# Optimization experiments

Measured on AMD Instinct MI355X. Metric: run time of the kernel, lower is better.

## Reference

```python
import jax, jax.numpy as jnp
import numpy as np

B, N1, N2, D, R = 4, 128, 128, 256, 4


def setup_inputs() -> dict:
    key = jax.random.key(0)
    ks = jax.random.split(key, 8)
    s = 0.02  # small init scale for weights
    return {
        "features1": jax.random.normal(ks[0], (B, N1, D), jnp.float32),
        "features2": jax.random.normal(ks[1], (B, N2, D), jnp.float32),
        # relation nets stacked over R: Linear(2D->D), Linear(D->D//2), Linear(D//2->1)
        "W1": jax.random.normal(ks[2], (R, 2 * D, D), jnp.float32) * s,
        "b1": jnp.zeros((R, D), jnp.float32),
        "W2": jax.random.normal(ks[3], (R, D, D // 2), jnp.float32) * s,
        "b2": jnp.zeros((R, D // 2), jnp.float32),
        "w3": jax.random.normal(ks[4], (R, D // 2), jnp.float32) * s,
        "b3": jnp.zeros((R,), jnp.float32),
        # aggregator: Linear(D*R -> 2D), Linear(2D -> D)
        "Wa1": jax.random.normal(ks[5], (D * R, 2 * D), jnp.float32) * s,
        "ba1": jnp.zeros((2 * D,), jnp.float32),
        "Wa2": jax.random.normal(ks[6], (2 * D, D), jnp.float32) * s,
        "ba2": jnp.zeros((D,), jnp.float32),
    }


def reference(features1, features2, W1, b1, W2, b2, w3, b3, Wa1, ba1, Wa2, ba2):
    b, n1, d = features1.shape
    n2 = features2.shape[1]
    r = W1.shape[0]
    # concat([f1_i, f2_j]) @ W1 == f1_i @ W1[:d] + f2_j @ W1[d:]
    W1a, W1b = W1[:, :d, :], W1[:, d:, :]
    h1 = jnp.einsum('bid,rde->brie', features1, W1a)          # [B,R,N1,D]
    h2 = jnp.einsum('bjd,rde->brje', features2, W1b)          # [B,R,N2,D]
    h = jax.nn.relu(h1[:, :, :, None, :] + h2[:, :, None, :, :]
                    + b1[None, :, None, None, :])             # [B,R,N1,N2,D]
    g = jax.nn.relu(jnp.einsum('brijd,rde->brije', h, W2)
                    + b2[None, :, None, None, :])             # [B,R,N1,N2,D//2]
    scores = jnp.einsum('brije,re->brij', g, w3) + b3[None, :, None, None]
    w = jax.nn.softmax(scores, axis=-1)                       # softmax over j (N2)
    rel = jnp.einsum('brij,bjd->brid', w, features2)          # [B,R,N1,D]
    # torch cat over relations along feature dim -> relation index outermost
    all_rel = rel.transpose(0, 2, 1, 3).reshape(b, n1, r * d)  # [B,N1,R*D]
    out = jax.nn.relu(all_rel @ Wa1 + ba1) @ Wa2 + ba2         # [B,N1,D]
    return out
```

## Files before the change

### kernel.cpp

```cpp
#include <hip/hip_runtime.h>


typedef _Float16 f16x8 __attribute__((ext_vector_type(8)));
typedef float f32x16 __attribute__((ext_vector_type(16)));

static __device__ __forceinline__ ushort to_h(float f) {
  _Float16 h = (_Float16)f;
  return __builtin_bit_cast(ushort, h);
}
static __device__ __forceinline__ uint pack2(float a, float b) {
  return (uint)to_h(a) | ((uint)to_h(b) << 16);
}
static __device__ __forceinline__ uint pk_add(uint a, uint b) {
  uint r;
  asm("v_pk_add_f16 %0, %1, %2" : "=v"(r) : "v"(a), "v"(b));
  return r;
}
static __device__ __forceinline__ uint pk_relu(uint a) {
  uint r;
  asm("v_pk_max_f16 %0, %1, %2" : "=v"(r) : "v"(a), "v"(0u));
  return r;
}

__global__ __launch_bounds__(256) void k_prep(
    const float* __restrict__ f1, const float* __restrict__ f2,
    const float* __restrict__ W1, const float* __restrict__ W2,
    const float* __restrict__ Wa1, const float* __restrict__ Wa2,
    uint* __restrict__ f1hp, uint* __restrict__ f2hp,
    ushort* __restrict__ W1swz, ushort* __restrict__ W2swz,
    ushort* __restrict__ f2swz, ushort* __restrict__ Wa1swz,
    ushort* __restrict__ Wa2swz)
{
  int blk = blockIdx.x, t = threadIdx.x;
  if (blk < 128) {
    int u = blk * 256 + t;
    float4 a = *(const float4*)&f1[u * 4];
    float4 b = *(const float4*)&f2[u * 4];
    *(uint2*)&f1hp[u * 2] = make_uint2(pack2(a.x, a.y), pack2(a.z, a.w));
    *(uint2*)&f2hp[u * 2] = make_uint2(pack2(b.x, b.y), pack2(b.z, b.w));
    return;
  }
  if (blk < 256) {
    int unit = blk - 128;
    int r = unit >> 5, half = (unit >> 4) & 1, ks = unit & 15;
    int l = t & 63, ctq = t >> 6;
    #pragma unroll
    for (int ci = 0; ci < 2; ++ci) {
      int ct = ctq + ci * 4;
      int e = ct * 32 + (l & 31);
      ushort us[8];
      #pragma unroll
      for (int j = 0; j < 8; ++j) {
        int d = ks * 16 + ((l >> 5) * 4) + (j & 3) + ((j >> 2) * 8);
        us[j] = to_h(W1[(size_t)(r * 512 + half * 256 + d) * 256 + e]);
      }
      uint4 pk;
      pk.x = (uint)us[0] | ((uint)us[1] << 16);
      pk.y = (uint)us[2] | ((uint)us[3] << 16);
      pk.z = (uint)us[4] | ((uint)us[5] << 16);
      pk.w = (uint)us[6] | ((uint)us[7] << 16);
      *(uint4*)&W1swz[(size_t)((((r * 2 + half) * 16 + ks) * 8 + ct) * 64 + l) * 8] = pk;
    }
    return;
  }
  if (blk < 272) {
    int sub = blk - 256;
    int r = sub >> 2, ks0 = (sub & 3) * 4;
    int ct = t >> 6, l = t & 63;
    #pragma unroll
    for (int ko = 0; ko < 4; ++ko) {
      int ks = ks0 + ko;
      ushort us[8];
      #pragma unroll
      for (int j = 0; j < 8; ++j) {
        int d = ks * 16 + ((j >> 2) * 8) + ((l >> 5) * 4) + (j & 3);
        int e = ct * 32 + (l & 31);
        us[j] = to_h(W2[(r * 256 + d) * 128 + e]);
      }
      uint4 pk;
      pk.x = (uint)us[0] | ((uint)us[1] << 16);
      pk.y = (uint)us[2] | ((uint)us[3] << 16);
      pk.z = (uint)us[4] | ((uint)us[5] << 16);
      pk.w = (uint)us[6] | ((uint)us[7] << 16);
      *(uint4*)&W2swz[(((r * 16 + ks) * 4 + ct) * 64 + l) * 8] = pk;
    }
    return;
  }
  if (blk < 288) {
    int sub = blk - 272;
    int w = t >> 6, l = t & 63;
    #pragma unroll
    for (int ko = 0; ko < 4; ++ko) {
      int u = sub * 16 + w * 4 + ko;
      int b = u >> 6, ks = (u >> 3) & 7, ctg = u & 7;
      ushort us[8];
      #pragma unroll
      for (int j = 0; j < 8; ++j) {
        int k = ks * 16 + ((l >> 5) * 4) + (j & 3) + ((j >> 2) * 8);
        int n = ctg * 32 + (l & 31);
        us[j] = to_h(f2[((size_t)b * 128 + k) * 256 + n]);
      }
      uint4 pk;
      pk.x = (uint)us[0] | ((uint)us[1] << 16);
      pk.y = (uint)us[2] | ((uint)us[3] << 16);
      pk.z = (uint)us[4] | ((uint)us[5] << 16);
      pk.w = (uint)us[6] | ((uint)us[7] << 16);
      *(uint4*)&f2swz[(((b * 8 + ks) * 8 + ctg) * 64 + l) * 8] = pk;
    }
    return;
  }
  if (blk < 304) {
    int sub = blk - 288;
    #pragma unroll
    for (int ko = 0; ko < 16; ++ko) {
      int id = sub * 4096 + ko * 256 + t;
      int ks = id >> 10, ct = (id >> 6) & 15, l = id & 63;
      ushort us[8];
      #pragma unroll
      for (int j = 0; j < 8; ++j) {
        int d = ks * 16 + ((l >> 5) * 4) + (j & 3) + ((j >> 2) * 8);
        int e = ct * 32 + (l & 31);
        us[j] = to_h(Wa1[(size_t)d * 512 + e]);
      }
      uint4 pk;
      pk.x = (uint)us[0] | ((uint)us[1] << 16);
      pk.y = (uint)us[2] | ((uint)us[3] << 16);
      pk.z = (uint)us[4] | ((uint)us[5] << 16);
      pk.w = (uint)us[6] | ((uint)us[7] << 16);
      *(uint4*)&Wa1swz[(size_t)id * 8] = pk;
    }
    return;
  }
  {
    int sub = blk - 304;
    #pragma unroll
    for (int ko = 0; ko < 4; ++ko) {
      int id = sub * 1024 + ko * 256 + t;
      int ks = id >> 9, ct = (id >> 6) & 7, l = id & 63;
      ushort us[8];
      #pragma unroll
      for (int j = 0; j < 8; ++j) {
        int d = ks * 16 + ((l >> 5) * 4) + (j & 3) + ((j >> 2) * 8);
        int e = ct * 32 + (l & 31);
        us[j] = to_h(Wa2[(size_t)d * 256 + e]);
      }
      uint4 pk;
      pk.x = (uint)us[0] | ((uint)us[1] << 16);
      pk.y = (uint)us[2] | ((uint)us[3] << 16);
      pk.z = (uint)us[4] | ((uint)us[5] << 16);
      pk.w = (uint)us[6] | ((uint)us[7] << 16);
      *(uint4*)&Wa2swz[(size_t)id * 8] = pk;
    }
    return;
  }
}

__global__ __launch_bounds__(256) void k_proj_mfma(
    const uint* __restrict__ f1hp, const uint* __restrict__ f2hp,
    const ushort* __restrict__ W1swz, const float* __restrict__ b1,
    ushort* __restrict__ h1p, ushort* __restrict__ h2)
{
  int bid = blockIdx.x;
  int it = bid & 3;
  int half = (bid >> 2) & 1;
  int r = (bid >> 3) & 3;
  int b = bid >> 5;
  int t = threadIdx.x, w = t >> 6, l = t & 63;
  __shared__ uint Au[32][132];

  const uint* src = (half ? f2hp : f1hp) + (size_t)b * 16384 + it * 32 * 128;
  #pragma unroll
  for (int q = 0; q < 4; ++q) {
    int lin = q * 256 + t;
    int row = lin >> 5, c4 = (lin & 31) * 4;
    *(uint4*)&Au[row][c4] = *(const uint4*)&src[row * 128 + c4];
  }
  __syncthreads();

  int m31 = l & 31, hi = l >> 5, hi2 = hi * 2;
  f32x16 acc0, acc1;
  #pragma unroll
  for (int e = 0; e < 16; ++e) { acc0[e] = 0.f; acc1[e] = 0.f; }

  const ushort* bb = W1swz + (size_t)(r * 2 + half) * 65536;
  for (int ks = 0; ks < 16; ++ks) {
    int u0 = ks * 8 + hi2;
    uint2 xa = *(const uint2*)&Au[m31][u0];
    uint2 xb = *(const uint2*)&Au[m31][u0 + 4];
    uint4 a4 = make_uint4(xa.x, xa.y, xb.x, xb.y);
    f16x8 af = __builtin_bit_cast(f16x8, a4);
    uint4 br0 = *(const uint4*)&bb[((ks * 8 + w * 2 + 0) * 64 + l) * 8];
    uint4 br1 = *(const uint4*)&bb[((ks * 8 + w * 2 + 1) * 64 + l) * 8];
    f16x8 bf0 = __builtin_bit_cast(f16x8, br0);
    f16x8 bf1 = __builtin_bit_cast(f16x8, br1);
    acc0 = __builtin_amdgcn_mfma_f32_32x32x16_f16(af, bf0, acc0, 0, 0, 0);
    acc1 = __builtin_amdgcn_mfma_f32_32x32x16_f16(af, bf1, acc1, 0, 0, 0);
  }

  ushort* ho = (half ? h2 : h1p) + ((size_t)((b * 4 + r) * 128 + it * 32)) * 256;
  #pragma unroll
  for (int ctl = 0; ctl < 2; ++ctl) {
    int e = (w * 2 + ctl) * 32 + m31;
    float bv = half ? 0.f : b1[r * 256 + e];
    #pragma unroll
    for (int g = 0; g < 16; ++g) {
      int row = (g & 3) + 8 * (g >> 2) + 4 * hi;
      ho[row * 256 + e] = to_h((ctl ? acc1[g] : acc0[g]) + bv);
    }
  }
}

__global__ __launch_bounds__(256, 4) void k_scores_mfma(
    const ushort* __restrict__ h1p, const ushort* __restrict__ h2,
    const ushort* __restrict__ W2swz, const float* __restrict__ b2,
    const float* __restrict__ w3, const float* __restrict__ b3,
    float* __restrict__ scores)
{
  int bid = blockIdx.x;
  int jt = bid & 7;
  int it = (bid >> 3) & 15;
  int r  = (bid >> 7) & 3;
  int b  = bid >> 9;
  int t = threadIdx.x, w = t >> 6, l = t & 63;
  __shared__ uint h1u[8][132];
  __shared__ uint h2u[16][132];
  __shared__ float xch[4][2][2][16];

  const uint* h1g = (const uint*)h1p + ((size_t)((b * 4 + r) * 128 + it * 8)) * 128;
  const uint* h2g = (const uint*)h2  + ((size_t)((b * 4 + r) * 128 + jt * 16)) * 128;
  {
    int row = t >> 5, c4 = (t & 31) * 4;
    *(uint4*)&h1u[row][c4] = *(const uint4*)&h1g[row * 128 + c4];
    *(uint4*)&h2u[row][c4] = *(const uint4*)&h2g[row * 128 + c4];
    *(uint4*)&h2u[row + 8][c4] = *(const uint4*)&h2g[(row + 8) * 128 + c4];
  }

  f32x16 acc[2][2];
  #pragma unroll
  for (int i = 0; i < 2; ++i)
    #pragma unroll
    for (int c = 0; c < 2; ++c)
      #pragma unroll
      for (int e = 0; e < 16; ++e) acc[i][c][e] = 0.f;

  int rtp = w & 1, ctp = w >> 1;
  int hi2 = (l >> 5) * 2;
  int m31 = l & 31;
  int jrow = m31 & 15;
  int irow0 = (rtp * 2 + 0) * 2 + (m31 >> 4);
  int irow1 = (rtp * 2 + 1) * 2 + (m31 >> 4);
  const ushort* bptr = W2swz + r * (16 * 4 * 64 * 8) + (((ctp * 2) * 64 + l) * 8);

  __syncthreads();

  const uint* h1r0 = &h1u[irow0][0];
  const uint* h1r1 = &h1u[irow1][0];
  const uint* h2r  = &h2u[jrow][0];
  uint4 nb0 = *(const uint4*)&bptr[0];
  uint4 nb1 = *(const uint4*)&bptr[512];
  #pragma unroll 2
  for (int ks = 0; ks < 16; ++ks) {
    uint4 b0 = nb0, b1 = nb1;
    if (ks < 15) {
      nb0 = *(const uint4*)&bptr[(ks + 1) * 2048];
      nb1 = *(const uint4*)&bptr[(ks + 1) * 2048 + 512];
    }
    int u0 = ks * 8 + hi2;
    uint2 ya  = *(const uint2*)&h2r[u0];
    uint2 yb  = *(const uint2*)&h2r[u0 + 4];
    uint2 xa0 = *(const uint2*)&h1r0[u0];
    uint2 xb0 = *(const uint2*)&h1r0[u0 + 4];
    uint2 xa1 = *(const uint2*)&h1r1[u0];
    uint2 xb1 = *(const uint2*)&h1r1[u0 + 4];
    uint4 pk0, pk1;
    pk0.x = pk_relu(pk_add(xa0.x, ya.x));
    pk0.y = pk_relu(pk_add(xa0.y, ya.y));
    pk0.z = pk_relu(pk_add(xb0.x, yb.x));
    pk0.w = pk_relu(pk_add(xb0.y, yb.y));
    pk1.x = pk_relu(pk_add(xa1.x, ya.x));
    pk1.y = pk_relu(pk_add(xa1.y, ya.y));
    pk1.z = pk_relu(pk_add(xb1.x, yb.x));
    pk1.w = pk_relu(pk_add(xb1.y, yb.y));
    f16x8 af0 = __builtin_bit_cast(f16x8, pk0);
    f16x8 af1 = __builtin_bit_cast(f16x8, pk1);
    f16x8 bf0 = __builtin_bit_cast(f16x8, b0);
    f16x8 bf1 = __builtin_bit_cast(f16x8, b1);
    acc[0][0] = __builtin_amdgcn_mfma_f32_32x32x16_f16(af0, bf0, acc[0][0], 0, 0, 0);
    acc[0][1] = __builtin_amdgcn_mfma_f32_32x32x16_f16(af0, bf1, acc[0][1], 0, 0, 0);
    acc[1][0] = __builtin_amdgcn_mfma_f32_32x32x16_f16(af1, bf0, acc[1][0], 0, 0, 0);
    acc[1][1] = __builtin_amdgcn_mfma_f32_32x32x16_f16(af1, bf1, acc[1][1], 0, 0, 0);
  }

  float sp[2][16];
  #pragma unroll
  for (int i = 0; i < 2; ++i)
    #pragma unroll
    for (int g = 0; g < 16; ++g) sp[i][g] = 0.f;
  #pragma unroll
  for (int ctl = 0; ctl < 2; ++ctl) {
    int e = (ctp * 2 + ctl) * 32 + m31;
    float w3v = w3[r * 128 + e];
    float b2v = b2[r * 128 + e];
    #pragma unroll
    for (int i = 0; i < 2; ++i)
      #pragma unroll
      for (int g = 0; g < 16; ++g)
        sp[i][g] = fmaf(w3v, fmaxf(acc[i][ctl][g] + b2v, 0.f), sp[i][g]);
  }
  #pragma unroll
  for (int off = 16; off >= 1; off >>= 1)
    #pragma unroll
    for (int i = 0; i < 2; ++i)
      #pragma unroll
      for (int g = 0; g < 16; ++g)
        sp[i][g] += __shfl_xor(sp[i][g], off, 64);
  int hi = l >> 5;
  if (m31 == 0) {
    #pragma unroll
    for (int i = 0; i < 2; ++i)
      #pragma unroll
      for (int g = 0; g < 16; ++g)
        xch[w][i][hi][g] = sp[i][g];
  }
  __syncthreads();
  if (w < 2 && m31 == 0) {
    float b3v = b3[r];
    float* sc_base = scores + (((b * 4 + r) * 128 + it * 8) * 128) + jt * 16;
    #pragma unroll
    for (int i = 0; i < 2; ++i)
      #pragma unroll
      for (int g = 0; g < 16; ++g) {
        float s = xch[w][i][hi][g] + xch[w + 2][i][hi][g] + b3v;
        int p = (w * 2 + i) * 32 + (g & 3) + 8 * (g >> 2) + hi * 4;
        sc_base[(p >> 4) * 128 + (p & 15)] = s;
      }
  }
}

__global__ __launch_bounds__(64, 1) void k_softrel_mfma(
    const float* __restrict__ scores, const ushort* __restrict__ f2swz,
    ushort* __restrict__ all_rel_h)
{
  int bid = blockIdx.x;
  int ctp  = bid & 1;
  int rowq = (bid >> 1) & 3;
  int nh   = (bid >> 3) & 1;
  int r    = (bid >> 4) & 3;
  int b    = bid >> 6;
  int l = threadIdx.x;
  int row = rowq * 32 + (l & 31);
  const float* srow = scores + ((size_t)(b * 4 + r) * 128 + row) * 128;

  float p[128];
  #pragma unroll
  for (int q = 0; q < 32; ++q) {
    float4 v = *(const float4*)&srow[q * 4];
    p[q * 4 + 0] = v.x; p[q * 4 + 1] = v.y;
    p[q * 4 + 2] = v.z; p[q * 4 + 3] = v.w;
  }
  float mm[8];
  #pragma unroll
  for (int c = 0; c < 8; ++c) mm[c] = p[c * 16];
  #pragma unroll
  for (int k = 1; k < 16; ++k)
    #pragma unroll
    for (int c = 0; c < 8; ++c) mm[c] = fmaxf(mm[c], p[c * 16 + k]);
  float m = fmaxf(fmaxf(fmaxf(mm[0], mm[1]), fmaxf(mm[2], mm[3])),
                  fmaxf(fmaxf(mm[4], mm[5]), fmaxf(mm[6], mm[7])));
  float ss[8];
  #pragma unroll
  for (int c = 0; c < 8; ++c) ss[c] = 0.f;
  #pragma unroll
  for (int k = 0; k < 16; ++k)
    #pragma unroll
    for (int c = 0; c < 8; ++c) {
      p[c * 16 + k] = __expf(p[c * 16 + k] - m);
      ss[c] += p[c * 16 + k];
    }
  float sum = ((ss[0] + ss[1]) + (ss[2] + ss[3])) + ((ss[4] + ss[5]) + (ss[6] + ss[7]));
  float inv = 1.f / sum;
  uint preg[64];
  #pragma unroll
  for (int q = 0; q < 64; ++q)
    preg[q] = pack2(p[2 * q] * inv, p[2 * q + 1] * inv);

  f32x16 acc[2];
  #pragma unroll
  for (int c = 0; c < 2; ++c)
    #pragma unroll
    for (int e = 0; e < 16; ++e) acc[c][e] = 0.f;

  int hi2 = (l >> 5) * 2;
  const ushort* bbase = f2swz + (size_t)b * (8 * 8 * 64 * 8);
  #pragma unroll
  for (int ks = 0; ks < 8; ++ks) {
    int b2i = ks * 8 + hi2;
    uint4 pk = make_uint4(preg[b2i], preg[b2i + 1], preg[b2i + 4], preg[b2i + 5]);
    f16x8 af = __builtin_bit_cast(f16x8, pk);
    #pragma unroll
    for (int ctl = 0; ctl < 2; ++ctl) {
      int ct = nh * 4 + ctp * 2 + ctl;
      uint4 braw = *(const uint4*)&bbase[((ks * 8 + ct) * 64 + l) * 8];
      f16x8 bfr = __builtin_bit_cast(f16x8, braw);
      acc[ctl] = __builtin_amdgcn_mfma_f32_32x32x16_f16(af, bfr, acc[ctl], 0, 0, 0);
    }
  }

  ushort* dst = all_rel_h + (size_t)(b * 128) * 1024;
  int ebase = r * 256 + nh * 128 + ctp * 64 + (l & 31);
  int half4 = (l >> 5) << 2;
  #pragma unroll
  for (int ctl = 0; ctl < 2; ++ctl)
    #pragma unroll
    for (int g = 0; g < 16; ++g) {
      int i = rowq * 32 + (g & 3) + 8 * (g >> 2) + half4;
      dst[(size_t)i * 1024 + ebase + ctl * 32] = to_h(acc[ctl][g]);
    }
}

__global__ __launch_bounds__(256) void k_mlp1(
    const ushort* __restrict__ all_rel_h, const ushort* __restrict__ Wa1swz,
    const float* __restrict__ ba1, ushort* __restrict__ hiddenh)
{
  int cq = blockIdx.x, rt = blockIdx.y;
  int t = threadIdx.x, w = t >> 6, l = t & 63;
  __shared__ uint Ah[32][514];
  const uint* Ag = (const uint*)all_rel_h + (size_t)rt * 32 * 512;
  #pragma unroll
  for (int q = 0; q < 16; ++q) {
    int lin = q * 256 + t;
    int row = lin >> 7, c4 = (lin & 127) * 4;
    *(uint4*)&Ah[row][c4] = *(const uint4*)&Ag[row * 512 + c4];
  }
  __syncthreads();

  int m31 = l & 31, hi = l >> 5, hi2 = hi * 2;
  int ct = cq * 4 + w;
  f32x16 acc;
  #pragma unroll
  for (int e = 0; e < 16; ++e) acc[e] = 0.f;
  for (int ks = 0; ks < 64; ++ks) {
    int u0 = ks * 8 + hi2;
    uint2 xa = *(const uint2*)&Ah[m31][u0];
    uint2 xb = *(const uint2*)&Ah[m31][u0 + 4];
    uint4 a4 = make_uint4(xa.x, xa.y, xb.x, xb.y);
    f16x8 af = __builtin_bit_cast(f16x8, a4);
    uint4 braw = *(const uint4*)&Wa1swz[(size_t)((ks * 16 + ct) * 64 + l) * 8];
    f16x8 bfr = __builtin_bit_cast(f16x8, braw);
    acc = __builtin_amdgcn_mfma_f32_32x32x16_f16(af, bfr, acc, 0, 0, 0);
  }
  int e = ct * 32 + m31;
  float bv = ba1[e];
  #pragma unroll
  for (int g = 0; g < 16; ++g) {
    int row = (g & 3) + 8 * (g >> 2) + 4 * hi;
    hiddenh[(size_t)(rt * 32 + row) * 512 + e] = to_h(fmaxf(acc[g] + bv, 0.f));
  }
}

__global__ __launch_bounds__(256) void k_mlp2(
    const ushort* __restrict__ hiddenh, const ushort* __restrict__ Wa2swz,
    const float* __restrict__ ba2, float* __restrict__ out)
{
  int cq = blockIdx.x, rt = blockIdx.y;
  int t = threadIdx.x, w = t >> 6, l = t & 63;
  __shared__ uint Ah[32][258];
  const uint* Ag = (const uint*)hiddenh + (size_t)rt * 32 * 256;
  #pragma unroll
  for (int q = 0; q < 8; ++q) {
    int lin = q * 256 + t;
    int row = lin >> 6, c4 = (lin & 63) * 4;
    *(uint4*)&Ah[row][c4] = *(const uint4*)&Ag[row * 256 + c4];
  }
  __syncthreads();

  int m31 = l & 31, hi = l >> 5, hi2 = hi * 2;
  int ct = cq * 4 + w;
  f32x16 acc;
  #pragma unroll
  for (int e = 0; e < 16; ++e) acc[e] = 0.f;
  for (int ks = 0; ks < 32; ++ks) {
    int u0 = ks * 8 + hi2;
    uint2 xa = *(const uint2*)&Ah[m31][u0];
    uint2 xb = *(const uint2*)&Ah[m31][u0 + 4];
    uint4 a4 = make_uint4(xa.x, xa.y, xb.x, xb.y);
    f16x8 af = __builtin_bit_cast(f16x8, a4);
    uint4 braw = *(const uint4*)&Wa2swz[(size_t)((ks * 8 + ct) * 64 + l) * 8];
    f16x8 bfr = __builtin_bit_cast(f16x8, braw);
    acc = __builtin_amdgcn_mfma_f32_32x32x16_f16(af, bfr, acc, 0, 0, 0);
  }
  int e = ct * 32 + m31;
  float bv = ba2[e];
  #pragma unroll
  for (int g = 0; g < 16; ++g) {
    int row = (g & 3) + 8 * (g >> 2) + 4 * hi;
    out[(size_t)(rt * 32 + row) * 256 + e] = acc[g] + bv;
  }
}

extern "C" void kernel_launch(void* const* d_in, const int* in_sizes, int n_in,
                              void* d_out, int out_size, void* d_ws, size_t ws_size,
                              hipStream_t stream) {
  const float* f1  = (const float*)d_in[0];
  const float* f2  = (const float*)d_in[1];
  const float* W1  = (const float*)d_in[2];
  const float* b1  = (const float*)d_in[3];
  const float* W2  = (const float*)d_in[4];
  const float* b2  = (const float*)d_in[5];
  const float* w3  = (const float*)d_in[6];
  const float* b3  = (const float*)d_in[7];
  const float* Wa1 = (const float*)d_in[8];
  const float* ba1 = (const float*)d_in[9];
  const float* Wa2 = (const float*)d_in[10];
  const float* ba2 = (const float*)d_in[11];
  float* out = (float*)d_out;
  float* ws = (float*)d_ws;

  uint*   f1hp     = (uint*)ws;
  uint*   f2hp     = (uint*)(ws + 65536);
  ushort* h1p      = (ushort*)(ws + 131072);
  ushort* h2       = (ushort*)(ws + 393216);
  float*  scores   = ws + 655360;
  ushort* all_relh = (ushort*)(ws + 917504);
  ushort* W1swz    = (ushort*)(ws + 1179648);
  ushort* W2swz    = (ushort*)(ws + 1441792);
  ushort* f2swz    = (ushort*)(ws + 1507328);
  ushort* Wa1swz   = (ushort*)(ws + 1572864);
  ushort* Wa2swz   = (ushort*)(ws + 1835008);
  ushort* hiddenh  = (ushort*)(ws + 1900544);

  hipLaunchKernelGGL(k_prep, dim3(320), dim3(256), 0, stream,
                     f1, f2, W1, W2, Wa1, Wa2,
                     f1hp, f2hp, W1swz, W2swz, f2swz, Wa1swz, Wa2swz);
  hipLaunchKernelGGL(k_proj_mfma, dim3(128), dim3(256), 0, stream,
                     f1hp, f2hp, W1swz, b1, h1p, h2);
  hipLaunchKernelGGL(k_scores_mfma, dim3(2048), dim3(256), 0, stream,
                     h1p, h2, W2swz, b2, w3, b3, scores);
  hipLaunchKernelGGL(k_softrel_mfma, dim3(256), dim3(64), 0, stream,
                     scores, f2swz, all_relh);
  hipLaunchKernelGGL(k_mlp1, dim3(4, 16), dim3(256), 0, stream,
                     all_relh, Wa1swz, ba1, hiddenh);
  hipLaunchKernelGGL(k_mlp2, dim3(2, 16), dim3(256), 0, stream,
                     hiddenh, Wa2swz, ba2, out);
}
```

Baseline: 62.35 us.

## Fuse input prep and W1 projection into one kernel reading fp32 directly

Merges the fp16 conversion and W1 swizzle steps into the projection kernel: the projection blocks now load fp32 features and W1 directly, pack them to fp16 on the fly, and run the MFMAs. This removes one kernel launch and the workspace round trip for the f1/f2 halves and the W1 swizzle. The cost is that W1 is read as scalar strided fp32 loads inside the MFMA loop instead of coalesced pre-swizzled uint4 loads. Each W1 slice is also re-read by the four it-blocks, and the other weight-prep blocks now share a launch with the heavier projection blocks.

```diff
diff --git a/kernel.cpp b/kernel.cpp
--- a/kernel.cpp
+++ b/kernel.cpp
@@ -22,49 +22,87 @@
   return r;
 }
 
-__global__ __launch_bounds__(256) void k_prep(
+__global__ __launch_bounds__(256) void k_prepproj(
     const float* __restrict__ f1, const float* __restrict__ f2,
-    const float* __restrict__ W1, const float* __restrict__ W2,
-    const float* __restrict__ Wa1, const float* __restrict__ Wa2,
-    uint* __restrict__ f1hp, uint* __restrict__ f2hp,
-    ushort* __restrict__ W1swz, ushort* __restrict__ W2swz,
-    ushort* __restrict__ f2swz, ushort* __restrict__ Wa1swz,
-    ushort* __restrict__ Wa2swz)
+    const float* __restrict__ W1, const float* __restrict__ b1,
+    const float* __restrict__ W2, const float* __restrict__ Wa1,
+    const float* __restrict__ Wa2,
+    ushort* __restrict__ W2swz, ushort* __restrict__ f2swz,
+    ushort* __restrict__ Wa1swz, ushort* __restrict__ Wa2swz,
+    ushort* __restrict__ h1p, ushort* __restrict__ h2)
 {
   int blk = blockIdx.x, t = threadIdx.x;
+  __shared__ uint Au[32][132];
+
   if (blk < 128) {
-    int u = blk * 256 + t;
-    float4 a = *(const float4*)&f1[u * 4];
-    float4 b = *(const float4*)&f2[u * 4];
-    *(uint2*)&f1hp[u * 2] = make_uint2(pack2(a.x, a.y), pack2(a.z, a.w));
-    *(uint2*)&f2hp[u * 2] = make_uint2(pack2(b.x, b.y), pack2(b.z, b.w));
+    int it = blk & 3;
+    int half = (blk >> 2) & 1;
+    int r = (blk >> 3) & 3;
+    int b = blk >> 5;
+    int w = t >> 6, l = t & 63;
+
+    const float* src = (half ? f2 : f1) + (size_t)b * 32768 + it * 32 * 256;
+    #pragma unroll
+    for (int q = 0; q < 4; ++q) {
+      int lin = q * 256 + t;
+      int row = lin >> 5;
+      int fo = (lin & 31) * 8;
+      float4 fa = *(const float4*)&src[row * 256 + fo];
+      float4 fb = *(const float4*)&src[row * 256 + fo + 4];
+      uint4 pk;
+      pk.x = pack2(fa.x, fa.y); pk.y = pack2(fa.z, fa.w);
+      pk.z = pack2(fb.x, fb.y); pk.w = pack2(fb.z, fb.w);
+      *(uint4*)&Au[row][(lin & 31) * 4] = pk;
+    }
+    __syncthreads();
+
+    int m31 = l & 31, hi = l >> 5, hi2 = hi * 2;
+    f32x16 acc0, acc1;
+    #pragma unroll
+    for (int e = 0; e < 16; ++e) { acc0[e] = 0.f; acc1[e] = 0.f; }
+
+    const float* W1b = W1 + (size_t)(r * 512 + half * 256) * 256;
+    int e0 = (w * 2 + 0) * 32 + m31;
+    int e1 = (w * 2 + 1) * 32 + m31;
+    for (int ks = 0; ks < 16; ++ks) {
+      int u0 = ks * 8 + hi2;
+      uint2 xa = *(const uint2*)&Au[m31][u0];
+      uint2 xb = *(const uint2*)&Au[m31][u0 + 4];
+      uint4 a4 = make_uint4(xa.x, xa.y, xb.x, xb.y);
+      f16x8 af = __builtin_bit_cast(f16x8, a4);
+      int d00 = ks * 16 + hi * 4;
+      const float* wr = W1b + (size_t)d00 * 256;
+      uint4 b0, b1;
+      b0.x = pack2(wr[0 * 256 + e0], wr[1 * 256 + e0]);
+      b0.y = pack2(wr[2 * 256 + e0], wr[3 * 256 + e0]);
+      b0.z = pack2(wr[8 * 256 + e0], wr[9 * 256 + e0]);
+      b0.w = pack2(wr[10 * 256 + e0], wr[11 * 256 + e0]);
+      b1.x = pack2(wr[0 * 256 + e1], wr[1 * 256 + e1]);
+      b1.y = pack2(wr[2 * 256 + e1], wr[3 * 256 + e1]);
+      b1.z = pack2(wr[8 * 256 + e1], wr[9 * 256 + e1]);
+      b1.w = pack2(wr[10 * 256 + e1], wr[11 * 256 + e1]);
+      f16x8 bf0 = __builtin_bit_cast(f16x8, b0);
+      f16x8 bf1 = __builtin_bit_cast(f16x8, b1);
+      acc0 = __builtin_amdgcn_mfma_f32_32x32x16_f16(af, bf0, acc0, 0, 0, 0);
+      acc1 = __builtin_amdgcn_mfma_f32_32x32x16_f16(af, bf1, acc1, 0, 0, 0);
+    }
+
+    ushort* ho = (half ? h2 : h1p) + ((size_t)((b * 4 + r) * 128 + it * 32)) * 256;
+    #pragma unroll
+    for (int ctl = 0; ctl < 2; ++ctl) {
+      int e = (w * 2 + ctl) * 32 + m31;
+      float bv = half ? 0.f : b1[r * 256 + e];
+      #pragma unroll
+      for (int g = 0; g < 16; ++g) {
+        int row = (g & 3) + 8 * (g >> 2) + 4 * hi;
+        ho[row * 256 + e] = to_h((ctl ? acc1[g] : acc0[g]) + bv);
+      }
+    }
     return;
   }
-  if (blk < 256) {
-    int unit = blk - 128;
-    int r = unit >> 5, half = (unit >> 4) & 1, ks = unit & 15;
-    int l = t & 63, ctq = t >> 6;
-    #pragma unroll
-    for (int ci = 0; ci < 2; ++ci) {
-      int ct = ctq + ci * 4;
-      int e = ct * 32 + (l & 31);
-      ushort us[8];
-      #pragma unroll
-      for (int j = 0; j < 8; ++j) {
-        int d = ks * 16 + ((l >> 5) * 4) + (j & 3) + ((j >> 2) * 8);
-        us[j] = to_h(W1[(size_t)(r * 512 + half * 256 + d) * 256 + e]);
-      }
-      uint4 pk;
-      pk.x = (uint)us[0] | ((uint)us[1] << 16);
-      pk.y = (uint)us[2] | ((uint)us[3] << 16);
-      pk.z = (uint)us[4] | ((uint)us[5] << 16);
-      pk.w = (uint)us[6] | ((uint)us[7] << 16);
-      *(uint4*)&W1swz[(size_t)((((r * 2 + half) * 16 + ks) * 8 + ct) * 64 + l) * 8] = pk;
-    }
-    return;
-  }
-  if (blk < 272) {
-    int sub = blk - 256;
+
+  if (blk < 144) {
+    int sub = blk - 128;
     int r = sub >> 2, ks0 = (sub & 3) * 4;
     int ct = t >> 6, l = t & 63;
     #pragma unroll
@@ -86,8 +124,8 @@
     }
     return;
   }
-  if (blk < 288) {
-    int sub = blk - 272;
+  if (blk < 160) {
+    int sub = blk - 144;
     int w = t >> 6, l = t & 63;
     #pragma unroll
     for (int ko = 0; ko < 4; ++ko) {
@@ -109,8 +147,8 @@
     }
     return;
   }
-  if (blk < 304) {
-    int sub = blk - 288;
+  if (blk < 176) {
+    int sub = blk - 160;
     #pragma unroll
     for (int ko = 0; ko < 16; ++ko) {
       int id = sub * 4096 + ko * 256 + t;
@@ -132,7 +170,7 @@
     return;
   }
   {
-    int sub = blk - 304;
+    int sub = blk - 176;
     #pragma unroll
     for (int ko = 0; ko < 4; ++ko) {
       int id = sub * 1024 + ko * 256 + t;
@@ -152,61 +190,6 @@
       *(uint4*)&Wa2swz[(size_t)id * 8] = pk;
     }
     return;
-  }
-}
-
-__global__ __launch_bounds__(256) void k_proj_mfma(
-    const uint* __restrict__ f1hp, const uint* __restrict__ f2hp,
-    const ushort* __restrict__ W1swz, const float* __restrict__ b1,
-    ushort* __restrict__ h1p, ushort* __restrict__ h2)
-{
-  int bid = blockIdx.x;
-  int it = bid & 3;
-  int half = (bid >> 2) & 1;
-  int r = (bid >> 3) & 3;
-  int b = bid >> 5;
-  int t = threadIdx.x, w = t >> 6, l = t & 63;
-  __shared__ uint Au[32][132];
-
-  const uint* src = (half ? f2hp : f1hp) + (size_t)b * 16384 + it * 32 * 128;
-  #pragma unroll
-  for (int q = 0; q < 4; ++q) {
-    int lin = q * 256 + t;
-    int row = lin >> 5, c4 = (lin & 31) * 4;
-    *(uint4*)&Au[row][c4] = *(const uint4*)&src[row * 128 + c4];
-  }
-  __syncthreads();
-
-  int m31 = l & 31, hi = l >> 5, hi2 = hi * 2;
-  f32x16 acc0, acc1;
-  #pragma unroll
-  for (int e = 0; e < 16; ++e) { acc0[e] = 0.f; acc1[e] = 0.f; }
-
-  const ushort* bb = W1swz + (size_t)(r * 2 + half) * 65536;
-  for (int ks = 0; ks < 16; ++ks) {
-    int u0 = ks * 8 + hi2;
-    uint2 xa = *(const uint2*)&Au[m31][u0];
-    uint2 xb = *(const uint2*)&Au[m31][u0 + 4];
-    uint4 a4 = make_uint4(xa.x, xa.y, xb.x, xb.y);
-    f16x8 af = __builtin_bit_cast(f16x8, a4);
-    uint4 br0 = *(const uint4*)&bb[((ks * 8 + w * 2 + 0) * 64 + l) * 8];
-    uint4 br1 = *(const uint4*)&bb[((ks * 8 + w * 2 + 1) * 64 + l) * 8];
-    f16x8 bf0 = __builtin_bit_cast(f16x8, br0);
-    f16x8 bf1 = __builtin_bit_cast(f16x8, br1);
-    acc0 = __builtin_amdgcn_mfma_f32_32x32x16_f16(af, bf0, acc0, 0, 0, 0);
-    acc1 = __builtin_amdgcn_mfma_f32_32x32x16_f16(af, bf1, acc1, 0, 0, 0);
-  }
-
-  ushort* ho = (half ? h2 : h1p) + ((size_t)((b * 4 + r) * 128 + it * 32)) * 256;
-  #pragma unroll
-  for (int ctl = 0; ctl < 2; ++ctl) {
-    int e = (w * 2 + ctl) * 32 + m31;
-    float bv = half ? 0.f : b1[r * 256 + e];
-    #pragma unroll
-    for (int g = 0; g < 16; ++g) {
-      int row = (g & 3) + 8 * (g >> 2) + 4 * hi;
-      ho[row * 256 + e] = to_h((ctl ? acc1[g] : acc0[g]) + bv);
-    }
   }
 }
 
@@ -516,24 +499,19 @@
   float* out = (float*)d_out;
   float* ws = (float*)d_ws;
 
-  uint*   f1hp     = (uint*)ws;
-  uint*   f2hp     = (uint*)(ws + 65536);
-  ushort* h1p      = (ushort*)(ws + 131072);
-  ushort* h2       = (ushort*)(ws + 393216);
-  float*  scores   = ws + 655360;
-  ushort* all_relh = (ushort*)(ws + 917504);
-  ushort* W1swz    = (ushort*)(ws + 1179648);
-  ushort* W2swz    = (ushort*)(ws + 1441792);
-  ushort* f2swz    = (ushort*)(ws + 1507328);
-  ushort* Wa1swz   = (ushort*)(ws + 1572864);
-  ushort* Wa2swz   = (ushort*)(ws + 1835008);
-  ushort* hiddenh  = (ushort*)(ws + 1900544);
-
-  hipLaunchKernelGGL(k_prep, dim3(320), dim3(256), 0, stream,
-                     f1, f2, W1, W2, Wa1, Wa2,
-                     f1hp, f2hp, W1swz, W2swz, f2swz, Wa1swz, Wa2swz);
-  hipLaunchKernelGGL(k_proj_mfma, dim3(128), dim3(256), 0, stream,
-                     f1hp, f2hp, W1swz, b1, h1p, h2);
+  ushort* h1p      = (ushort*)ws;
+  ushort* h2       = (ushort*)(ws + 262144);
+  float*  scores   = ws + 524288;
+  ushort* all_relh = (ushort*)(ws + 786432);
+  ushort* W2swz    = (ushort*)(ws + 1048576);
+  ushort* f2swz    = (ushort*)(ws + 1114112);
+  ushort* Wa1swz   = (ushort*)(ws + 1179648);
+  ushort* Wa2swz   = (ushort*)(ws + 1441792);
+  ushort* hiddenh  = (ushort*)(ws + 1507328);
+
+  hipLaunchKernelGGL(k_prepproj, dim3(192), dim3(256), 0, stream,
+                     f1, f2, W1, b1, W2, Wa1, Wa2,
+                     W2swz, f2swz, Wa1swz, Wa2swz, h1p, h2);
   hipLaunchKernelGGL(k_scores_mfma, dim3(2048), dim3(256), 0, stream,
                      h1p, h2, W2swz, b2, w3, b3, scores);
   hipLaunchKernelGGL(k_softrel_mfma, dim3(256), dim3(64), 0, stream,
```

Measured after the change: 61.50 us. Within noise of the previous version (-1.4%).
